# Kernel tuning notes

Measured on AMD Instinct MI355X. Metric: run time of the kernel, lower is better.

## Reference

```python
import math
import jax
import jax.numpy as jnp
import numpy as np

SEGMENT_SIZE = 2048   # w (init: segment_size)
DILATION_RATE = 4     # r (init: dilation_rate)
D_MODEL = 1024        # init: d_model


def _sparse_indices(n: int, w: int, r: int, head_idx: int) -> np.ndarray:
    """Static SparsifyIndices: per segment of size w, take tokens offset::r.
    Since r divides w, every segment yields exactly m=w//r indices (no -1 pad).
    Returns flat global token indices, shape (S*m,)."""
    S = n // w
    m = w // r
    off = head_idx % r
    seg_start = np.arange(S, dtype=np.int64)[:, None] * w      # (S,1)
    within = off + r * np.arange(m, dtype=np.int64)[None, :]   # (1,m)
    return (seg_start + within).reshape(-1)


def setup_inputs() -> dict:
    key = jax.random.key(0)
    x = jax.random.normal(key, (4, 8192, D_MODEL), dtype=jnp.float32)
    return {"x": x, "head_idx": 1}


def reference(x, head_idx):
    b, n0, d = x.shape
    w, r = SEGMENT_SIZE, DILATION_RATE
    pad = (-n0) % w
    if pad:
        x = jnp.pad(x, ((0, 0), (0, pad), (0, 0)))
    n = n0 + pad
    idx = _sparse_indices(n, w, r, int(head_idx))  # static, (S*m,)
    S, m = n // w, w // r

    # Gather dilated tokens per segment: (b, S, m, d)
    xg = x[:, idx, :].reshape(b, S, m, d)

    # Softmax attention within each sub-segment (q=k=v=xg)
    scores = jnp.einsum('bsid,bsjd->bsij', xg, xg) / math.sqrt(d)  # (b,S,m,m)
    probs = jax.nn.softmax(scores, axis=-1)
    att = jnp.einsum('bsij,bsjd->bsid', probs, xg).reshape(b, S * m, d)

    # MixOutputs: alpha-weighted scatter-add back to full sequence
    denoms = att.sum(-1)                                       # (b, S*m)
    denom_sums = jnp.zeros((b, n), x.dtype).at[:, idx].add(denoms)
    alphas = denoms / denom_sums[:, idx]                       # (b, S*m)
    out = jnp.zeros((b, n, d), x.dtype).at[:, idx, :].add(att * alphas[..., None])
    return out
```

## Files before the change

kernel.cpp:

```cpp
#include <hip/hip_runtime.h>
#include <hip/hip_bf16.h>


typedef __bf16 bf16_t;
typedef __bf16 bf16x8 __attribute__((ext_vector_type(8)));
typedef float floatx4 __attribute__((ext_vector_type(4)));

#define D_MODEL 1024
#define SEG_W   2048
#define RATE    4
#define M_SUB   512
#define NTOK    8192
#define NSEGT   16
#define XG_ELEMS ((long)NSEGT * M_SUB * D_MODEL)
#define QK_SCALE 0.17677669529663689f

__device__ __forceinline__ void gload16(const bf16_t* g, bf16_t* l) {
    __builtin_amdgcn_global_load_lds(
        (const __attribute__((address_space(1))) void*)g,
        (__attribute__((address_space(3))) void*)l, 16, 0, 0);
}

__global__ __launch_bounds__(256) void gather_kernel(
    const float* __restrict__ x, const int* __restrict__ hidp,
    bf16_t* __restrict__ xg, bf16_t* __restrict__ xgT)
{
    const int off = ((hidp[0] % RATE) + RATE) % RATE;
    const int bid = blockIdx.x;
    const int seg = bid >> 7;
    const int rem = bid & 127;
    const int it  = rem >> 4;
    const int dt  = rem & 15;
    const int b   = seg >> 2, s = seg & 3;

    __shared__ ushort tile[64][65];

    const int t  = threadIdx.x;
    const int r  = t >> 2;
    const int cq = (t & 3) << 4;

    union U8 { bf16x8 v; ushort u[8]; };

    {
        const int  i   = it * 64 + r;
        const long tok = (long)s * SEG_W + off + 4L * i;
        const float* src = x + ((long)b * NTOK + tok) * D_MODEL + dt * 64 + cq;
        float4 f0 = ((const float4*)src)[0];
        float4 f1 = ((const float4*)src)[1];
        float4 f2 = ((const float4*)src)[2];
        float4 f3 = ((const float4*)src)[3];
        U8 lo, hi, ls, hs;
        lo.v[0]=(bf16_t)f0.x; lo.v[1]=(bf16_t)f0.y; lo.v[2]=(bf16_t)f0.z; lo.v[3]=(bf16_t)f0.w;
        lo.v[4]=(bf16_t)f1.x; lo.v[5]=(bf16_t)f1.y; lo.v[6]=(bf16_t)f1.z; lo.v[7]=(bf16_t)f1.w;
        hi.v[0]=(bf16_t)f2.x; hi.v[1]=(bf16_t)f2.y; hi.v[2]=(bf16_t)f2.z; hi.v[3]=(bf16_t)f2.w;
        hi.v[4]=(bf16_t)f3.x; hi.v[5]=(bf16_t)f3.y; hi.v[6]=(bf16_t)f3.z; hi.v[7]=(bf16_t)f3.w;
        ls.v[0]=(bf16_t)(f0.x*QK_SCALE); ls.v[1]=(bf16_t)(f0.y*QK_SCALE);
        ls.v[2]=(bf16_t)(f0.z*QK_SCALE); ls.v[3]=(bf16_t)(f0.w*QK_SCALE);
        ls.v[4]=(bf16_t)(f1.x*QK_SCALE); ls.v[5]=(bf16_t)(f1.y*QK_SCALE);
        ls.v[6]=(bf16_t)(f1.z*QK_SCALE); ls.v[7]=(bf16_t)(f1.w*QK_SCALE);
        hs.v[0]=(bf16_t)(f2.x*QK_SCALE); hs.v[1]=(bf16_t)(f2.y*QK_SCALE);
        hs.v[2]=(bf16_t)(f2.z*QK_SCALE); hs.v[3]=(bf16_t)(f2.w*QK_SCALE);
        hs.v[4]=(bf16_t)(f3.x*QK_SCALE); hs.v[5]=(bf16_t)(f3.y*QK_SCALE);
        hs.v[6]=(bf16_t)(f3.z*QK_SCALE); hs.v[7]=(bf16_t)(f3.w*QK_SCALE);
        bf16_t* dstg = xg + ((long)seg * M_SUB + i) * D_MODEL + dt * 64 + cq;
        *(bf16x8*)(dstg)     = ls.v;
        *(bf16x8*)(dstg + 8) = hs.v;
        #pragma unroll
        for (int j = 0; j < 8; ++j) { tile[r][cq + j] = lo.u[j]; tile[r][cq + 8 + j] = hi.u[j]; }
    }
    __syncthreads();
    {
        const int dc = r;
        const int iq = cq;
        U8 o0, o1;
        #pragma unroll
        for (int j = 0; j < 8; ++j) { o0.u[j] = tile[iq + j][dc]; o1.u[j] = tile[iq + 8 + j][dc]; }
        bf16_t* dstT = xgT + ((long)seg * D_MODEL + dt * 64 + dc) * M_SUB + it * 64 + iq;
        *(bf16x8*)(dstT)     = o0.v;
        *(bf16x8*)(dstT + 8) = o1.v;
    }
}

__global__ __launch_bounds__(512) void qk_kernel(
    const bf16_t* __restrict__ xg, bf16_t* __restrict__ S)
{
    const int bid = blockIdx.x;
    const int seg = bid >> 5;
    const int mt  = (bid >> 2) & 7;
    const int nt  = bid & 3;

    const int tid  = threadIdx.x;
    const int w    = tid >> 6;
    const int lane = tid & 63;
    const int l16  = lane & 15;
    const int quad = lane >> 4;
    const int wr   = w >> 2, wc = w & 3;
    const int row8 = lane >> 3;
    const int cswz = ((lane & 7) ^ row8) * 8;
    const int rsw  = l16 & 7;

    __shared__ alignas(16) bf16_t As[64 * 64];
    __shared__ alignas(16) bf16_t Bs[128 * 64];

    const bf16_t* xseg = xg + (long)seg * M_SUB * D_MODEL;

    const bf16_t* ga  = xseg + (long)(mt * 64 + w * 8 + row8) * D_MODEL + cswz;
    const bf16_t* gb0 = xseg + (long)(nt * 128 + w * 16 + row8) * D_MODEL + cswz;
    const bf16_t* gb1 = gb0 + 8 * D_MODEL;
    bf16_t* la  = &As[(w * 8) * 64];
    bf16_t* lb0 = &Bs[(w * 16 + 0) * 64];
    bf16_t* lb1 = &Bs[(w * 16 + 8) * 64];

    floatx4 acc[2][2];
    #pragma unroll
    for (int i = 0; i < 2; ++i)
        #pragma unroll
        for (int j = 0; j < 2; ++j) acc[i][j] = (floatx4){0.f, 0.f, 0.f, 0.f};

    for (int kk = 0; kk < D_MODEL; kk += 64) {
        __syncthreads();
        gload16(ga  + kk, la);
        gload16(gb0 + kk, lb0); gload16(gb1 + kk, lb1);
        __syncthreads();

        #pragma unroll
        for (int ks = 0; ks < 2; ++ks) {
            bf16x8 Af[2], Bf[2];
            #pragma unroll
            for (int m2 = 0; m2 < 2; ++m2) {
                const int row = wr * 32 + m2 * 16 + l16;
                Af[m2] = *(const bf16x8*)&As[row * 64 + (((ks * 4 + quad) ^ rsw) * 8)];
            }
            #pragma unroll
            for (int n2 = 0; n2 < 2; ++n2) {
                const int row = wc * 32 + n2 * 16 + l16;
                Bf[n2] = *(const bf16x8*)&Bs[row * 64 + (((ks * 4 + quad) ^ rsw) * 8)];
            }
            #pragma unroll
            for (int m2 = 0; m2 < 2; ++m2)
                #pragma unroll
                for (int n2 = 0; n2 < 2; ++n2)
                    acc[m2][n2] = __builtin_amdgcn_mfma_f32_16x16x32_bf16(Af[m2], Bf[n2], acc[m2][n2], 0, 0, 0);
        }
    }

    bf16_t* Sseg = S + (long)seg * M_SUB * M_SUB;
    #pragma unroll
    for (int m2 = 0; m2 < 2; ++m2) {
        const int qrow = mt * 64 + wr * 32 + m2 * 16 + quad * 4;
        #pragma unroll
        for (int n2 = 0; n2 < 2; ++n2) {
            const int col = nt * 128 + wc * 32 + n2 * 16 + l16;
            #pragma unroll
            for (int rg = 0; rg < 4; ++rg)
                Sseg[(long)(qrow + rg) * M_SUB + col] = (bf16_t)acc[m2][n2][rg];
        }
    }
}

__global__ __launch_bounds__(256) void softmax_kernel(bf16_t* __restrict__ S)
{
    const int row  = blockIdx.x * 4 + (threadIdx.x >> 6);
    const int lane = threadIdx.x & 63;
    bf16_t* p = S + (long)row * M_SUB + lane * 8;
    bf16x8 v = *(const bf16x8*)p;
    float f[8];
    #pragma unroll
    for (int j = 0; j < 8; ++j) f[j] = (float)v[j];
    float m = f[0];
    #pragma unroll
    for (int j = 1; j < 8; ++j) m = fmaxf(m, f[j]);
    #pragma unroll
    for (int d = 1; d < 64; d <<= 1) m = fmaxf(m, __shfl_xor(m, d, 64));
    float sum = 0.f;
    #pragma unroll
    for (int j = 0; j < 8; ++j) { f[j] = __expf(f[j] - m); sum += f[j]; }
    #pragma unroll
    for (int d = 1; d < 64; d <<= 1) sum += __shfl_xor(sum, d, 64);
    const float inv = 1.0f / sum;
    #pragma unroll
    for (int j = 0; j < 8; ++j) v[j] = (bf16_t)(f[j] * inv);
    *(bf16x8*)p = v;
}

__global__ __launch_bounds__(512) void pv_kernel(
    const bf16_t* __restrict__ P, const bf16_t* __restrict__ xgT,
    const int* __restrict__ hidp, float* __restrict__ out)
{
    const int off = ((hidp[0] % RATE) + RATE) % RATE;
    const int bid = blockIdx.x;
    const int seg = bid >> 5;
    const int mt  = (bid >> 3) & 3;
    const int nt  = bid & 7;
    const int b   = seg >> 2, s = seg & 3;

    const int tid  = threadIdx.x;
    const int w    = tid >> 6;
    const int lane = tid & 63;
    const int l16  = lane & 15;
    const int quad = lane >> 4;
    const int wr   = w >> 1, wc = w & 1;
    const int row8 = lane >> 3;
    const int cswz = ((lane & 7) ^ row8) * 8;
    const int rsw  = l16 & 7;

    __shared__ alignas(16) bf16_t As[128 * 64];
    __shared__ alignas(16) bf16_t Bs[128 * 64];

    const bf16_t* Aseg = P   + (long)seg * M_SUB * M_SUB  + (long)mt * 128 * M_SUB;
    const bf16_t* Bseg = xgT + (long)seg * D_MODEL * M_SUB + (long)nt * 128 * M_SUB;

    const bf16_t* ga0 = Aseg + (long)(w * 16 + row8) * M_SUB + cswz;
    const bf16_t* ga1 = ga0 + 8 * M_SUB;
    const bf16_t* gb0 = Bseg + (long)(w * 16 + row8) * M_SUB + cswz;
    const bf16_t* gb1 = gb0 + 8 * M_SUB;
    bf16_t* la0 = &As[(w * 16 + 0) * 64];
    bf16_t* la1 = &As[(w * 16 + 8) * 64];
    bf16_t* lb0 = &Bs[(w * 16 + 0) * 64];
    bf16_t* lb1 = &Bs[(w * 16 + 8) * 64];

    floatx4 acc[2][4];
    #pragma unroll
    for (int i = 0; i < 2; ++i)
        #pragma unroll
        for (int j = 0; j < 4; ++j) acc[i][j] = (floatx4){0.f, 0.f, 0.f, 0.f};

    for (int kk = 0; kk < M_SUB; kk += 64) {
        __syncthreads();
        gload16(ga0 + kk, la0); gload16(ga1 + kk, la1);
        gload16(gb0 + kk, lb0); gload16(gb1 + kk, lb1);
        __syncthreads();

        #pragma unroll
        for (int ks = 0; ks < 2; ++ks) {
            bf16x8 Af[2], Bf[4];
            #pragma unroll
            for (int m2 = 0; m2 < 2; ++m2) {
                const int row = wr * 32 + m2 * 16 + l16;
                Af[m2] = *(const bf16x8*)&As[row * 64 + (((ks * 4 + quad) ^ rsw) * 8)];
            }
            #pragma unroll
            for (int n2 = 0; n2 < 4; ++n2) {
                const int row = wc * 64 + n2 * 16 + l16;
                Bf[n2] = *(const bf16x8*)&Bs[row * 64 + (((ks * 4 + quad) ^ rsw) * 8)];
            }
            #pragma unroll
            for (int m2 = 0; m2 < 2; ++m2)
                #pragma unroll
                for (int n2 = 0; n2 < 4; ++n2)
                    acc[m2][n2] = __builtin_amdgcn_mfma_f32_16x16x32_bf16(Af[m2], Bf[n2], acc[m2][n2], 0, 0, 0);
        }
    }

    float* obase = out + (long)b * NTOK * D_MODEL;
    #pragma unroll
    for (int m2 = 0; m2 < 2; ++m2) {
        const int qrow0 = mt * 128 + wr * 32 + m2 * 16 + quad * 4;
        #pragma unroll
        for (int rg = 0; rg < 4; ++rg) {
            const long tok = (long)s * SEG_W + off + 4L * (qrow0 + rg);
            float* orow = obase + tok * D_MODEL;
            #pragma unroll
            for (int n2 = 0; n2 < 4; ++n2) {
                const int d = nt * 128 + wc * 64 + n2 * 16 + l16;
                __builtin_nontemporal_store(acc[m2][n2][rg], &orow[d]);
            }
        }
    }

    {
        const floatx4 z = {0.f, 0.f, 0.f, 0.f};
        const int zr = tid >> 5;
        const int zc = tid & 31;
        #pragma unroll 4
        for (int p = 0; p < 24; ++p) {
            const int j = p * 16 + zr;
            const int q = j / 3, e = j % 3;
            const int delta = e + (e >= off ? 1 : 0);
            const long tok = (long)s * SEG_W + 4L * (mt * 128 + q) + delta;
            float* dst = obase + tok * D_MODEL + nt * 128 + zc * 4;
            __builtin_nontemporal_store(z, (floatx4*)dst);
        }
    }
}

extern "C" void kernel_launch(void* const* d_in, const int* in_sizes, int n_in,
                              void* d_out, int out_size, void* d_ws, size_t ws_size,
                              hipStream_t stream) {
    const float* x   = (const float*)d_in[0];
    const int*   hid = (const int*)d_in[1];
    float*       out = (float*)d_out;
    bf16_t* xg  = (bf16_t*)d_ws;
    bf16_t* xgT = xg + XG_ELEMS;
    bf16_t* S   = xgT + XG_ELEMS;

    gather_kernel<<<dim3(2048), dim3(256), 0, stream>>>(x, hid, xg, xgT);
    qk_kernel<<<dim3(512), dim3(512), 0, stream>>>(xg, S);
    softmax_kernel<<<dim3(2048), dim3(256), 0, stream>>>(S);
    pv_kernel<<<dim3(512), dim3(512), 0, stream>>>(S, xgT, hid, out);
}
```

Before: 250.1 us.

## Fuse softmax into QK kernel with full-row tiles and apply scale in exp

Merges the QK^T GEMM and the row softmax into one kernel. Each block computes 32 full query rows against all 512 keys, reducing max and sum across waves through shared memory before writing normalized probabilities. This removes the separate softmax launch and the round trip of the score matrix through global memory. The gather no longer stores a pre-scaled copy, and the scale is applied inside the exponent instead. The trade-off is half as many blocks and a larger LDS footprint per block, which lowers parallelism in the GEMM.

```diff
diff --git a/kernel.cpp b/kernel.cpp
--- a/kernel.cpp
+++ b/kernel.cpp
@@ -13,7 +13,7 @@
 #define NTOK    8192
 #define NSEGT   16
 #define XG_ELEMS ((long)NSEGT * M_SUB * D_MODEL)
-#define QK_SCALE 0.17677669529663689f
+#define SM_SCALE 0.03125f
 
 __device__ __forceinline__ void gload16(const bf16_t* g, bf16_t* l) {
     __builtin_amdgcn_global_load_lds(
@@ -49,22 +49,14 @@
         float4 f1 = ((const float4*)src)[1];
         float4 f2 = ((const float4*)src)[2];
         float4 f3 = ((const float4*)src)[3];
-        U8 lo, hi, ls, hs;
+        U8 lo, hi;
         lo.v[0]=(bf16_t)f0.x; lo.v[1]=(bf16_t)f0.y; lo.v[2]=(bf16_t)f0.z; lo.v[3]=(bf16_t)f0.w;
         lo.v[4]=(bf16_t)f1.x; lo.v[5]=(bf16_t)f1.y; lo.v[6]=(bf16_t)f1.z; lo.v[7]=(bf16_t)f1.w;
         hi.v[0]=(bf16_t)f2.x; hi.v[1]=(bf16_t)f2.y; hi.v[2]=(bf16_t)f2.z; hi.v[3]=(bf16_t)f2.w;
         hi.v[4]=(bf16_t)f3.x; hi.v[5]=(bf16_t)f3.y; hi.v[6]=(bf16_t)f3.z; hi.v[7]=(bf16_t)f3.w;
-        ls.v[0]=(bf16_t)(f0.x*QK_SCALE); ls.v[1]=(bf16_t)(f0.y*QK_SCALE);
-        ls.v[2]=(bf16_t)(f0.z*QK_SCALE); ls.v[3]=(bf16_t)(f0.w*QK_SCALE);
-        ls.v[4]=(bf16_t)(f1.x*QK_SCALE); ls.v[5]=(bf16_t)(f1.y*QK_SCALE);
-        ls.v[6]=(bf16_t)(f1.z*QK_SCALE); ls.v[7]=(bf16_t)(f1.w*QK_SCALE);
-        hs.v[0]=(bf16_t)(f2.x*QK_SCALE); hs.v[1]=(bf16_t)(f2.y*QK_SCALE);
-        hs.v[2]=(bf16_t)(f2.z*QK_SCALE); hs.v[3]=(bf16_t)(f2.w*QK_SCALE);
-        hs.v[4]=(bf16_t)(f3.x*QK_SCALE); hs.v[5]=(bf16_t)(f3.y*QK_SCALE);
-        hs.v[6]=(bf16_t)(f3.z*QK_SCALE); hs.v[7]=(bf16_t)(f3.w*QK_SCALE);
         bf16_t* dstg = xg + ((long)seg * M_SUB + i) * D_MODEL + dt * 64 + cq;
-        *(bf16x8*)(dstg)     = ls.v;
-        *(bf16x8*)(dstg + 8) = hs.v;
+        *(bf16x8*)(dstg)     = lo.v;
+        *(bf16x8*)(dstg + 8) = hi.v;
         #pragma unroll
         for (int j = 0; j < 8; ++j) { tile[r][cq + j] = lo.u[j]; tile[r][cq + 8 + j] = hi.u[j]; }
     }
@@ -81,106 +73,146 @@
     }
 }
 
-__global__ __launch_bounds__(512) void qk_kernel(
-    const bf16_t* __restrict__ xg, bf16_t* __restrict__ S)
+__global__ __launch_bounds__(512) void qks_kernel(
+    const bf16_t* __restrict__ xg, bf16_t* __restrict__ P)
 {
     const int bid = blockIdx.x;
-    const int seg = bid >> 5;
-    const int mt  = (bid >> 2) & 7;
-    const int nt  = bid & 3;
+    const int seg = bid >> 4;
+    const int mt  = bid & 15;
 
     const int tid  = threadIdx.x;
     const int w    = tid >> 6;
     const int lane = tid & 63;
     const int l16  = lane & 15;
     const int quad = lane >> 4;
-    const int wr   = w >> 2, wc = w & 3;
     const int row8 = lane >> 3;
     const int cswz = ((lane & 7) ^ row8) * 8;
     const int rsw  = l16 & 7;
 
-    __shared__ alignas(16) bf16_t As[64 * 64];
-    __shared__ alignas(16) bf16_t Bs[128 * 64];
+    __shared__ alignas(16) bf16_t As[32 * 64];
+    __shared__ alignas(16) bf16_t Bs[512 * 64];
+    __shared__ float redm[8][32];
+    __shared__ float reds[8][32];
 
     const bf16_t* xseg = xg + (long)seg * M_SUB * D_MODEL;
 
-    const bf16_t* ga  = xseg + (long)(mt * 64 + w * 8 + row8) * D_MODEL + cswz;
-    const bf16_t* gb0 = xseg + (long)(nt * 128 + w * 16 + row8) * D_MODEL + cswz;
-    const bf16_t* gb1 = gb0 + 8 * D_MODEL;
-    bf16_t* la  = &As[(w * 8) * 64];
-    bf16_t* lb0 = &Bs[(w * 16 + 0) * 64];
-    bf16_t* lb1 = &Bs[(w * 16 + 8) * 64];
-
-    floatx4 acc[2][2];
+    const bf16_t* gb = xseg + (long)(w * 64 + row8) * D_MODEL + cswz;
+    const bf16_t* ga = xseg + (long)(mt * 32 + (w & 3) * 8 + row8) * D_MODEL + cswz;
+    bf16_t* lb = &Bs[(w * 64) * 64];
+    bf16_t* la = &As[((w & 3) * 8) * 64];
+
+    floatx4 acc[2][4];
     #pragma unroll
     for (int i = 0; i < 2; ++i)
         #pragma unroll
-        for (int j = 0; j < 2; ++j) acc[i][j] = (floatx4){0.f, 0.f, 0.f, 0.f};
+        for (int j = 0; j < 4; ++j) acc[i][j] = (floatx4){0.f, 0.f, 0.f, 0.f};
 
     for (int kk = 0; kk < D_MODEL; kk += 64) {
         __syncthreads();
-        gload16(ga  + kk, la);
-        gload16(gb0 + kk, lb0); gload16(gb1 + kk, lb1);
+        #pragma unroll
+        for (int rr = 0; rr < 8; ++rr)
+            gload16(gb + (long)rr * 8 * D_MODEL + kk, lb + rr * 8 * 64);
+        if (w < 4) gload16(ga + kk, la);
         __syncthreads();
 
         #pragma unroll
         for (int ks = 0; ks < 2; ++ks) {
-            bf16x8 Af[2], Bf[2];
+            bf16x8 Af[2], Bf[4];
             #pragma unroll
             for (int m2 = 0; m2 < 2; ++m2) {
-                const int row = wr * 32 + m2 * 16 + l16;
+                const int row = m2 * 16 + l16;
                 Af[m2] = *(const bf16x8*)&As[row * 64 + (((ks * 4 + quad) ^ rsw) * 8)];
             }
             #pragma unroll
-            for (int n2 = 0; n2 < 2; ++n2) {
-                const int row = wc * 32 + n2 * 16 + l16;
-                Bf[n2] = *(const bf16x8*)&Bs[row * 64 + (((ks * 4 + quad) ^ rsw) * 8)];
+            for (int n2 = 0; n2 < 4; ++n2) {
+                const int key = w * 64 + n2 * 16 + l16;
+                Bf[n2] = *(const bf16x8*)&Bs[key * 64 + (((ks * 4 + quad) ^ rsw) * 8)];
             }
             #pragma unroll
             for (int m2 = 0; m2 < 2; ++m2)
                 #pragma unroll
-                for (int n2 = 0; n2 < 2; ++n2)
+                for (int n2 = 0; n2 < 4; ++n2)
                     acc[m2][n2] = __builtin_amdgcn_mfma_f32_16x16x32_bf16(Af[m2], Bf[n2], acc[m2][n2], 0, 0, 0);
         }
     }
 
-    bf16_t* Sseg = S + (long)seg * M_SUB * M_SUB;
+    float mx[2][4];
+    #pragma unroll
+    for (int m2 = 0; m2 < 2; ++m2)
+        #pragma unroll
+        for (int rg = 0; rg < 4; ++rg) {
+            float m = fmaxf(fmaxf(acc[m2][0][rg], acc[m2][1][rg]),
+                            fmaxf(acc[m2][2][rg], acc[m2][3][rg]));
+            #pragma unroll
+            for (int d = 1; d < 16; d <<= 1) m = fmaxf(m, __shfl_xor(m, d, 64));
+            mx[m2][rg] = m;
+        }
+    if (l16 == 0) {
+        #pragma unroll
+        for (int m2 = 0; m2 < 2; ++m2)
+            #pragma unroll
+            for (int rg = 0; rg < 4; ++rg)
+                redm[w][m2 * 16 + quad * 4 + rg] = mx[m2][rg];
+    }
+    __syncthreads();
+    float M[2][4], sm[2][4];
+    #pragma unroll
+    for (int m2 = 0; m2 < 2; ++m2)
+        #pragma unroll
+        for (int rg = 0; rg < 4; ++rg) {
+            const int rr = m2 * 16 + quad * 4 + rg;
+            float m = redm[0][rr];
+            #pragma unroll
+            for (int w2 = 1; w2 < 8; ++w2) m = fmaxf(m, redm[w2][rr]);
+            M[m2][rg] = m;
+            sm[m2][rg] = 0.f;
+        }
+    #pragma unroll
+    for (int m2 = 0; m2 < 2; ++m2)
+        #pragma unroll
+        for (int n2 = 0; n2 < 4; ++n2)
+            #pragma unroll
+            for (int rg = 0; rg < 4; ++rg) {
+                float p = __expf((acc[m2][n2][rg] - M[m2][rg]) * SM_SCALE);
+                acc[m2][n2][rg] = p;
+                sm[m2][rg] += p;
+            }
+    #pragma unroll
+    for (int m2 = 0; m2 < 2; ++m2)
+        #pragma unroll
+        for (int rg = 0; rg < 4; ++rg) {
+            float s2 = sm[m2][rg];
+            #pragma unroll
+            for (int d = 1; d < 16; d <<= 1) s2 += __shfl_xor(s2, d, 64);
+            sm[m2][rg] = s2;
+        }
+    if (l16 == 0) {
+        #pragma unroll
+        for (int m2 = 0; m2 < 2; ++m2)
+            #pragma unroll
+            for (int rg = 0; rg < 4; ++rg)
+                reds[w][m2 * 16 + quad * 4 + rg] = sm[m2][rg];
+    }
+    __syncthreads();
+
+    bf16_t* Pseg = P + (long)seg * M_SUB * M_SUB;
     #pragma unroll
     for (int m2 = 0; m2 < 2; ++m2) {
-        const int qrow = mt * 64 + wr * 32 + m2 * 16 + quad * 4;
-        #pragma unroll
-        for (int n2 = 0; n2 < 2; ++n2) {
-            const int col = nt * 128 + wc * 32 + n2 * 16 + l16;
-            #pragma unroll
-            for (int rg = 0; rg < 4; ++rg)
-                Sseg[(long)(qrow + rg) * M_SUB + col] = (bf16_t)acc[m2][n2][rg];
-        }
-    }
-}
-
-__global__ __launch_bounds__(256) void softmax_kernel(bf16_t* __restrict__ S)
-{
-    const int row  = blockIdx.x * 4 + (threadIdx.x >> 6);
-    const int lane = threadIdx.x & 63;
-    bf16_t* p = S + (long)row * M_SUB + lane * 8;
-    bf16x8 v = *(const bf16x8*)p;
-    float f[8];
-    #pragma unroll
-    for (int j = 0; j < 8; ++j) f[j] = (float)v[j];
-    float m = f[0];
-    #pragma unroll
-    for (int j = 1; j < 8; ++j) m = fmaxf(m, f[j]);
-    #pragma unroll
-    for (int d = 1; d < 64; d <<= 1) m = fmaxf(m, __shfl_xor(m, d, 64));
-    float sum = 0.f;
-    #pragma unroll
-    for (int j = 0; j < 8; ++j) { f[j] = __expf(f[j] - m); sum += f[j]; }
-    #pragma unroll
-    for (int d = 1; d < 64; d <<= 1) sum += __shfl_xor(sum, d, 64);
-    const float inv = 1.0f / sum;
-    #pragma unroll
-    for (int j = 0; j < 8; ++j) v[j] = (bf16_t)(f[j] * inv);
-    *(bf16x8*)p = v;
+        #pragma unroll
+        for (int rg = 0; rg < 4; ++rg) {
+            const int rr = m2 * 16 + quad * 4 + rg;
+            float s2 = reds[0][rr];
+            #pragma unroll
+            for (int w2 = 1; w2 < 8; ++w2) s2 += reds[w2][rr];
+            const float inv = 1.0f / s2;
+            const int qrow = mt * 32 + rr;
+            #pragma unroll
+            for (int n2 = 0; n2 < 4; ++n2) {
+                const int col = w * 64 + n2 * 16 + l16;
+                Pseg[(long)qrow * M_SUB + col] = (bf16_t)(acc[m2][n2][rg] * inv);
+            }
+        }
+    }
 }
 
 __global__ __launch_bounds__(512) void pv_kernel(
@@ -292,10 +324,9 @@
     float*       out = (float*)d_out;
     bf16_t* xg  = (bf16_t*)d_ws;
     bf16_t* xgT = xg + XG_ELEMS;
-    bf16_t* S   = xgT + XG_ELEMS;
+    bf16_t* P   = xgT + XG_ELEMS;
 
     gather_kernel<<<dim3(2048), dim3(256), 0, stream>>>(x, hid, xg, xgT);
-    qk_kernel<<<dim3(512), dim3(512), 0, stream>>>(xg, S);
-    softmax_kernel<<<dim3(2048), dim3(256), 0, stream>>>(S);
-    pv_kernel<<<dim3(512), dim3(512), 0, stream>>>(S, xgT, hid, out);
-}
+    qks_kernel<<<dim3(256), dim3(512), 0, stream>>>(xg, P);
+    pv_kernel<<<dim3(512), dim3(512), 0, stream>>>(P, xgT, hid, out);
+}
```

Result: slower. 259.6 us (+3.8%).
